# Performance work log

Hardware: AMD Instinct MI355X
Metric: run time of the kernel (lower is better)

## Reference

```python
import jax, jax.numpy as jnp
import numpy as np

EMBED_DIM = 768
NUM_HEADS = 12
SEGMENT_LENGTHS = (2048, 4096, 8192)
DILATION_RATES = (1, 2, 4)
LN_EPS = 1e-5


def setup_inputs() -> dict:
    key = jax.random.key(0)
    ks = jax.random.split(key, 12)
    B, N, E = 2, 8192, EMBED_DIM
    xavier = (2.0 / (E + E)) ** 0.5  # xavier_normal_ std for square weight
    return {
        "query": jax.random.normal(ks[0], (B, N, E), jnp.float32),
        "key_": jax.random.normal(ks[1], (B, N, E), jnp.float32),
        "value": jax.random.normal(ks[2], (B, N, E), jnp.float32),
        "Wq": jax.random.normal(ks[3], (E, E), jnp.float32) * xavier,
        "bq": jnp.zeros((E,), jnp.float32),
        "Wk": jax.random.normal(ks[4], (E, E), jnp.float32) * xavier,
        "bk": jnp.zeros((E,), jnp.float32),
        "Wv": jax.random.normal(ks[5], (E, E), jnp.float32) * xavier,
        "bv": jnp.zeros((E,), jnp.float32),
        "Wo": jax.random.normal(ks[6], (E, E), jnp.float32) * xavier,
        "bo": jnp.zeros((E,), jnp.float32),
        "ln_g": jnp.ones((E,), jnp.float32),
        "ln_b": jnp.zeros((E,), jnp.float32),
    }


def _dilated_attention(q, k, v):
    # q,k,v: [b, n, h, d]  (LongNet dilated attention, non-causal)
    b, n, h, d = q.shape
    G = len(SEGMENT_LENGTHS)
    hpg = h // G  # heads per dilation group
    scale = 1.0 / jnp.sqrt(jnp.asarray(d, q.dtype))
    out = jnp.zeros_like(q)
    for i, (g, r) in enumerate(zip(SEGMENT_LENGTHS, DILATION_RATES)):
        offset = i % r
        hmin, hmax = i * hpg, (i + 1) * hpg
        def seg(x):
            # [b, n_seg, g, h, d] -> dilate within segment, slice head group
            xs = x.reshape(b, n // g, g, h, d)
            return xs[:, :, offset::r, hmin:hmax, :]  # [b, ns, s, hg, d]
        qs, ks_, vs = seg(q), seg(k), seg(v)
        # attention within each dilated segment
        scores = jnp.einsum("bnshd,bnthd->bnhst", qs, ks_) * scale
        attn = jax.nn.softmax(scores, axis=-1)
        xo = jnp.einsum("bnhst,bnthd->bnshd", attn, vs)
        out_r = out.reshape(b, n // g, g, h, d)
        out_r = out_r.at[:, :, offset::r, hmin:hmax, :].add(xo)
        out = out_r.reshape(b, n, h, d)
    return out / G


def reference(query, key_, value, Wq, bq, Wk, bk, Wv, bv, Wo, bo, ln_g, ln_b):
    b, n, e = query.shape
    h, d = NUM_HEADS, e // NUM_HEADS
    q = (query @ Wq.T + bq).reshape(b, n, h, d)
    k = (key_ @ Wk.T + bk).reshape(b, n, h, d)
    v = (value @ Wv.T + bv).reshape(b, n, h, d)
    x = _dilated_attention(q, k, v).reshape(b, n, e)
    mu = jnp.mean(x, axis=-1, keepdims=True)
    var = jnp.mean(jnp.square(x - mu), axis=-1, keepdims=True)
    x = (x - mu) * jax.lax.rsqrt(var + LN_EPS) * ln_g + ln_b
    return x @ Wo.T + bo
```

## Files before the change

kernel.cpp:

```cpp
#include <hip/hip_runtime.h>
#include <hip/hip_bf16.h>
#include <stdint.h>

typedef unsigned int uint32;
typedef unsigned short u16;
typedef __attribute__((ext_vector_type(4))) float f32x4;
typedef __attribute__((ext_vector_type(16))) float f32x16;
typedef __attribute__((ext_vector_type(8))) __bf16 bf16x8;
typedef __attribute__((ext_vector_type(8))) short i16x8;
typedef __attribute__((ext_vector_type(4))) short i16x4;
typedef __attribute__((ext_vector_type(4))) uint32 u32x4;

#define DEVINL static __device__ __forceinline__

DEVINL u16 f2bf(float f){
  uint32 u = __builtin_bit_cast(uint32, f);
  return (u16)((u + 0x7fffu + ((u >> 16) & 1u)) >> 16);
}

DEVINL uint32 cvtpk(float lo, float hi){
  uint32 r;
  asm("v_cvt_pk_bf16_f32 %0, %1, %2" : "=v"(r) : "v"(lo), "v"(hi));
  return r;
}

DEVINL void permswap(uint32 &a, uint32 &b){
  asm volatile("s_nop 1\n\tv_permlane32_swap_b32 %0, %1" : "+v"(a), "+v"(b));
}

DEVINL f32x4 mfma16(bf16x8 a, bf16x8 b, f32x4 c){
  return __builtin_amdgcn_mfma_f32_16x16x32_bf16(a, b, c, 0, 0, 0);
}
DEVINL f32x16 mfma32(bf16x8 a, bf16x8 b, f32x16 c){
  return __builtin_amdgcn_mfma_f32_32x32x16_bf16(a, b, c, 0, 0, 0);
}
DEVINL f32x16 zero16(){
  f32x16 z;
  #pragma unroll
  for (int r = 0; r < 16; ++r) z[r] = 0.f;
  return z;
}

DEVINL void gload16(const u16* g, u16* l){
  __builtin_amdgcn_global_load_lds(
      (const __attribute__((address_space(1))) uint32*)g,
      (__attribute__((address_space(3))) uint32*)l, 16, 0, 0);
}

static constexpr int LDK = 40;
static constexpr size_t ISTR = 2048 * 64;
static constexpr float QSCALE = 0.18033688011112042f;

__global__ void cvt_w(const float* __restrict__ src, u16* __restrict__ dst, int n4){
  int i = blockIdx.x * 256 + threadIdx.x;
  if (i < n4){
    f32x4 v = *(const f32x4*)(src + (size_t)i * 4);
    u16 o[4];
    #pragma unroll
    for (int j = 0; j < 4; ++j) o[j] = f2bf(v[j]);
    *(i16x4*)(dst + (size_t)i * 4) = *(const i16x4*)o;
  }
}

__global__ __launch_bounds__(256) void qkv_gemm(
    const float* __restrict__ X, const u16* __restrict__ W,
    const float* __restrict__ bias, u16* __restrict__ Yg,
    float scale, int tmode)
{
  __shared__ u16 As[128 * LDK];
  __shared__ u16 Bs[128 * LDK];
  const int tid = threadIdx.x;
  const int l = tid & 63, w = tid >> 6;
  const int l15 = l & 15, lh = l >> 4;
  const int wr = w >> 1, wc = w & 1;
  const int row0 = blockIdx.x * 128, col0 = blockIdx.y * 128;
  const int sr = tid >> 1, skc = (tid & 1) * 16;

  const float* ap = X + (size_t)(row0 + sr) * 768 + skc;
  const u16*   bp = W + (size_t)(col0 + sr) * 768 + skc;

  f32x4 acc[4][4];
  #pragma unroll
  for (int i = 0; i < 4; ++i)
    #pragma unroll
    for (int j = 0; j < 4; ++j) acc[i][j] = f32x4{0.f, 0.f, 0.f, 0.f};

  f32x4 ra0, ra1, ra2, ra3; i16x8 rb0, rb1;
  ra0 = *(const f32x4*)(ap);      ra1 = *(const f32x4*)(ap + 4);
  ra2 = *(const f32x4*)(ap + 8);  ra3 = *(const f32x4*)(ap + 12);
  rb0 = *(const i16x8*)(bp);      rb1 = *(const i16x8*)(bp + 8);

  for (int ks = 0; ks < 24; ++ks) {
    __syncthreads();
    u32x4 w0 = { cvtpk(ra0[0], ra0[1]), cvtpk(ra0[2], ra0[3]),
                 cvtpk(ra1[0], ra1[1]), cvtpk(ra1[2], ra1[3]) };
    u32x4 w1 = { cvtpk(ra2[0], ra2[1]), cvtpk(ra2[2], ra2[3]),
                 cvtpk(ra3[0], ra3[1]), cvtpk(ra3[2], ra3[3]) };
    *(i16x8*)&As[sr * LDK + skc]     = __builtin_bit_cast(i16x8, w0);
    *(i16x8*)&As[sr * LDK + skc + 8] = __builtin_bit_cast(i16x8, w1);
    *(i16x8*)&Bs[sr * LDK + skc]     = rb0;
    *(i16x8*)&Bs[sr * LDK + skc + 8] = rb1;
    __syncthreads();
    if (ks < 23) {
      const float* ap2 = ap + (ks + 1) * 32;
      const u16*   bp2 = bp + (ks + 1) * 32;
      ra0 = *(const f32x4*)(ap2);      ra1 = *(const f32x4*)(ap2 + 4);
      ra2 = *(const f32x4*)(ap2 + 8);  ra3 = *(const f32x4*)(ap2 + 12);
      rb0 = *(const i16x8*)(bp2);      rb1 = *(const i16x8*)(bp2 + 8);
    }
    bf16x8 af[4], bfr[4];
    #pragma unroll
    for (int mi = 0; mi < 4; ++mi)
      af[mi] = *(const bf16x8*)&As[(wr * 64 + mi * 16 + l15) * LDK + lh * 8];
    #pragma unroll
    for (int ni = 0; ni < 4; ++ni)
      bfr[ni] = *(const bf16x8*)&Bs[(wc * 64 + ni * 16 + l15) * LDK + lh * 8];
    #pragma unroll
    for (int mi = 0; mi < 4; ++mi)
      #pragma unroll
      for (int ni = 0; ni < 4; ++ni)
        acc[mi][ni] = mfma16(af[mi], bfr[ni], acc[mi][ni]);
  }

  #pragma unroll
  for (int ni = 0; ni < 4; ++ni) {
    const int e = col0 + wc * 64 + ni * 16 + l15;
    const int h = e >> 6, d = e & 63;
    const int grp = h >> 2, hg = h & 3;
    const int instB = (grp == 0) ? 0 : (grp == 1) ? 32 : 48;
    const float bia = bias[e];
    #pragma unroll
    for (int mi = 0; mi < 4; ++mi) {
      #pragma unroll
      for (int r = 0; r < 4; ++r) {
        const int row = row0 + wr * 64 + mi * 16 + lh * 4 + r;
        const int b = row >> 13, nn = row & 8191;
        const int p = nn & ((2048 << grp) - 1);
        if ((p & ((1 << grp) - 1)) != grp) continue;
        const int seg = nn >> (11 + grp);
        const int t = (p - grp) >> grp;
        const int inst = instB + ((b * (4 >> grp) + seg) << 2) + hg;
        const u16 val = f2bf((acc[mi][ni][r] + bia) * scale);
        if (tmode == 0) Yg[(size_t)inst * ISTR + (size_t)t * 64 + d] = val;
        else            Yg[(size_t)inst * ISTR + (size_t)d * 2048 + t] = val;
      }
    }
  }
}

__global__ __launch_bounds__(256) void dil_attn(
    const u16* __restrict__ Qg, const u16* __restrict__ Kg,
    const u16* __restrict__ VgT, uint32* __restrict__ Op32, float* __restrict__ Ls)
{
  __shared__ u16 Kb[2][64 * 64];
  __shared__ u16 Vb[2][64 * 64];
  const int tid = threadIdx.x;
  const int w = tid >> 6, l = tid & 63;
  const int l31 = l & 31, hi = l >> 5;
  const int id = blockIdx.x;
  const int nid = (id & 7) * 224 + (id >> 3);
  const int inst = nid >> 5, rem = nid & 31;
  const int qb = rem >> 1, kh = rem & 1;
  const size_t ibase = (size_t)inst * ISTR;
  const int qbase = qb * 128 + w * 32;
  const int k0base = kh * 1024;

  const u16* qlane = Qg + ibase + (size_t)(qbase + l31) * 64 + hi * 8;
  const bf16x8 qf0 = *(const bf16x8*)(qlane);
  const bf16x8 qf1 = *(const bf16x8*)(qlane + 16);
  const bf16x8 qf2 = *(const bf16x8*)(qlane + 32);
  const bf16x8 qf3 = *(const bf16x8*)(qlane + 48);

  const int srow = l >> 3;
  const int scol = ((l & 7) ^ (srow & 7)) << 3;
  const u16* kgs = Kg  + ibase + (size_t)srow * 64 + scol;
  const u16* vgs = VgT + ibase + (size_t)srow * 2048 + scol;

  f32x16 acc0 = zero16(), acc1 = zero16(), rs = zero16();
  const int sxor = (l31 & 7) << 3;
  const bf16x8 ones = __builtin_bit_cast(bf16x8,
      u32x4{0x3F803F80u, 0x3F803F80u, 0x3F803F80u, 0x3F803F80u});

  auto STAGE = [&](int buf, int k0){
    #pragma unroll
    for (int q = 0; q < 2; ++q){
      const int rb = w * 16 + q * 8;
      gload16(kgs + (size_t)(k0 + rb) * 64, &Kb[buf][rb * 64]);
      gload16(vgs + (size_t)rb * 2048 + k0, &Vb[buf][rb * 64]);
    }
  };

  STAGE(0, k0base);
  asm volatile("s_waitcnt vmcnt(0)");
  __syncthreads();

  int cur = 0;
  for (int step = 0; step < 16; ++step) {
    if (step < 15) STAGE(cur ^ 1, k0base + ((step + 1) << 6));
    const u16* kt = &Kb[cur][0];
    const u16* vt = &Vb[cur][0];
    #pragma unroll
    for (int s = 0; s < 2; ++s) {
      const int ksub = s * 32;
      const int krow = (ksub + l31) * 64;
      bf16x8 kc0 = *(const bf16x8*)&kt[krow + ((hi * 8)      ^ sxor)];
      bf16x8 kc1 = *(const bf16x8*)&kt[krow + ((16 + hi * 8) ^ sxor)];
      bf16x8 kc2 = *(const bf16x8*)&kt[krow + ((32 + hi * 8) ^ sxor)];
      bf16x8 kc3 = *(const bf16x8*)&kt[krow + ((48 + hi * 8) ^ sxor)];

      f32x16 sT = zero16();
      sT = mfma32(kc0, qf0, sT);
      sT = mfma32(kc1, qf1, sT);
      sT = mfma32(kc2, qf2, sT);
      sT = mfma32(kc3, qf3, sT);

      #pragma unroll
      for (int r = 0; r < 16; ++r) sT[r] = __builtin_amdgcn_exp2f(sT[r]);

      uint32 cw0 = cvtpk(sT[0],  sT[1]),  cw1 = cvtpk(sT[2],  sT[3]);
      uint32 cw2 = cvtpk(sT[4],  sT[5]),  cw3 = cvtpk(sT[6],  sT[7]);
      uint32 cw4 = cvtpk(sT[8],  sT[9]),  cw5 = cvtpk(sT[10], sT[11]);
      uint32 cw6 = cvtpk(sT[12], sT[13]), cw7 = cvtpk(sT[14], sT[15]);
      permswap(cw0, cw2); permswap(cw1, cw3);
      permswap(cw4, cw6); permswap(cw5, cw7);
      bf16x8 pa0 = __builtin_bit_cast(bf16x8, u32x4{cw0, cw1, cw2, cw3});
      bf16x8 pa1 = __builtin_bit_cast(bf16x8, u32x4{cw4, cw5, cw6, cw7});

      const int vr0 = l31 * 64, vr1 = (l31 + 32) * 64;
      bf16x8 v00 = *(const bf16x8*)&vt[vr0 + ((ksub + hi * 8)      ^ sxor)];
      bf16x8 v01 = *(const bf16x8*)&vt[vr0 + ((ksub + 16 + hi * 8) ^ sxor)];
      bf16x8 v10 = *(const bf16x8*)&vt[vr1 + ((ksub + hi * 8)      ^ sxor)];
      bf16x8 v11 = *(const bf16x8*)&vt[vr1 + ((ksub + 16 + hi * 8) ^ sxor)];

      rs   = mfma32(pa0, ones, rs);
      rs   = mfma32(pa1, ones, rs);
      acc0 = mfma32(pa0, v00, acc0);
      acc0 = mfma32(pa1, v01, acc0);
      acc1 = mfma32(pa0, v10, acc1);
      acc1 = mfma32(pa1, v11, acc1);
    }
    asm volatile("s_waitcnt vmcnt(0)");
    __syncthreads();
    cur ^= 1;
  }

  if (l31 == 0) {
    float* lsp = Ls + ((size_t)kh * 56 + inst) * 2048 + qbase;
    #pragma unroll
    for (int r = 0; r < 16; ++r) {
      const int qrow = (r & 3) + 8 * (r >> 2) + 4 * hi;
      lsp[qrow] = rs[r];
    }
  }
  uint32* op = Op32 + (size_t)kh * (56u * 2048u * 32u)
                    + ((size_t)inst * 2048 + qbase) * 32 + l31;
  #pragma unroll
  for (int r = 0; r < 16; ++r) {
    const int qrow = (r & 3) + 8 * (r >> 2) + 4 * hi;
    op[(size_t)qrow * 32] = cvtpk(acc0[r], acc1[r]);
  }
}

__global__ __launch_bounds__(256) void ln_gather(
    const uint32* __restrict__ Op32, const float* __restrict__ Ls,
    const float* __restrict__ gamma, const float* __restrict__ beta,
    u16* __restrict__ xln)
{
  const int row = blockIdx.x;
  const int b = row >> 13, nn = row & 8191;
  const int tid = threadIdx.x;
  const size_t KHOFF = 56u * 2048u * 32u;
  float v[3];
  #pragma unroll
  for (int j = 0; j < 3; ++j) {
    const int e = tid + j * 256;
    const int h = e >> 6, d = e & 63;
    const int grp = h >> 2, hg = h & 3;
    const int p = nn & ((2048 << grp) - 1);
    float val = 0.f;
    if ((p & ((1 << grp) - 1)) == grp) {
      const int seg = nn >> (11 + grp);
      const int instB = (grp == 0) ? 0 : (grp == 1) ? 32 : 48;
      const int inst = instB + ((b * (4 >> grp) + seg) << 2) + hg;
      const int t = (p - grp) >> grp;
      const size_t wbase = ((size_t)inst * 2048 + t) * 32 + (d & 31);
      const uint32 w0 = Op32[wbase];
      const uint32 w1 = Op32[wbase + KHOFF];
      const float o0 = __builtin_bit_cast(float, d < 32 ? (w0 << 16) : (w0 & 0xFFFF0000u));
      const float o1 = __builtin_bit_cast(float, d < 32 ? (w1 << 16) : (w1 & 0xFFFF0000u));
      const float s = Ls[(size_t)inst * 2048 + t] + Ls[(size_t)(56 * 2048) + inst * 2048 + t];
      val = (o0 + o1) * (1.0f / (3.0f * s));
    }
    v[j] = val;
  }
  float s = v[0] + v[1] + v[2];
  float q = v[0]*v[0] + v[1]*v[1] + v[2]*v[2];
  #pragma unroll
  for (int off = 1; off < 64; off <<= 1) { s += __shfl_xor(s, off); q += __shfl_xor(q, off); }
  __shared__ float red[8];
  const int w = tid >> 6, l = tid & 63;
  if (l == 0) { red[w] = s; red[4 + w] = q; }
  __syncthreads();
  s = red[0] + red[1] + red[2] + red[3];
  q = red[4] + red[5] + red[6] + red[7];
  const float mu = s * (1.f / 768.f);
  const float var = q * (1.f / 768.f) - mu * mu;
  const float rs = rsqrtf(var + 1e-5f);
  #pragma unroll
  for (int j = 0; j < 3; ++j) {
    const int e = tid + j * 256;
    xln[(size_t)row * 768 + e] = f2bf((v[j] - mu) * rs * gamma[e] + beta[e]);
  }
}

__global__ __launch_bounds__(256) void out_gemm(
    const u16* __restrict__ Xb, const u16* __restrict__ W,
    const float* __restrict__ bias, float* __restrict__ out)
{
  __shared__ u16 As[128 * LDK];
  __shared__ u16 Bs[128 * LDK];
  const int tid = threadIdx.x;
  const int l = tid & 63, w = tid >> 6;
  const int l15 = l & 15, lh = l >> 4;
  const int wr = w >> 1, wc = w & 1;
  const int row0 = blockIdx.x * 128, col0 = blockIdx.y * 128;
  const int sr = tid >> 1, skc = (tid & 1) * 16;

  const u16* ap = Xb + (size_t)(row0 + sr) * 768 + skc;
  const u16* bp = W + (size_t)(col0 + sr) * 768 + skc;

  f32x4 acc[4][4];
  #pragma unroll
  for (int i = 0; i < 4; ++i)
    #pragma unroll
    for (int j = 0; j < 4; ++j) acc[i][j] = f32x4{0.f, 0.f, 0.f, 0.f};

  i16x8 ra0, ra1, rb0, rb1;
  ra0 = *(const i16x8*)(ap); ra1 = *(const i16x8*)(ap + 8);
  rb0 = *(const i16x8*)(bp); rb1 = *(const i16x8*)(bp + 8);

  for (int ks = 0; ks < 24; ++ks) {
    __syncthreads();
    *(i16x8*)&As[sr * LDK + skc]     = ra0;
    *(i16x8*)&As[sr * LDK + skc + 8] = ra1;
    *(i16x8*)&Bs[sr * LDK + skc]     = rb0;
    *(i16x8*)&Bs[sr * LDK + skc + 8] = rb1;
    __syncthreads();
    if (ks < 23) {
      const u16* ap2 = ap + (ks + 1) * 32;
      const u16* bp2 = bp + (ks + 1) * 32;
      ra0 = *(const i16x8*)(ap2); ra1 = *(const i16x8*)(ap2 + 8);
      rb0 = *(const i16x8*)(bp2); rb1 = *(const i16x8*)(bp2 + 8);
    }
    bf16x8 af[4], bfr[4];
    #pragma unroll
    for (int mi = 0; mi < 4; ++mi)
      af[mi] = *(const bf16x8*)&As[(wr * 64 + mi * 16 + l15) * LDK + lh * 8];
    #pragma unroll
    for (int ni = 0; ni < 4; ++ni)
      bfr[ni] = *(const bf16x8*)&Bs[(wc * 64 + ni * 16 + l15) * LDK + lh * 8];
    #pragma unroll
    for (int mi = 0; mi < 4; ++mi)
      #pragma unroll
      for (int ni = 0; ni < 4; ++ni)
        acc[mi][ni] = mfma16(af[mi], bfr[ni], acc[mi][ni]);
  }

  #pragma unroll
  for (int ni = 0; ni < 4; ++ni) {
    const int e = col0 + wc * 64 + ni * 16 + l15;
    const float bia = bias[e];
    #pragma unroll
    for (int mi = 0; mi < 4; ++mi) {
      #pragma unroll
      for (int r = 0; r < 4; ++r) {
        const int row = row0 + wr * 64 + mi * 16 + lh * 4 + r;
        out[(size_t)row * 768 + e] = acc[mi][ni][r] + bia;
      }
    }
  }
}

extern "C" void kernel_launch(void* const* d_in, const int* in_sizes, int n_in,
                              void* d_out, int out_size, void* d_ws, size_t ws_size,
                              hipStream_t stream) {
  const float* query = (const float*)d_in[0];
  const float* key_  = (const float*)d_in[1];
  const float* value = (const float*)d_in[2];
  const float* Wq = (const float*)d_in[3];
  const float* bq = (const float*)d_in[4];
  const float* Wk = (const float*)d_in[5];
  const float* bk = (const float*)d_in[6];
  const float* Wv = (const float*)d_in[7];
  const float* bv = (const float*)d_in[8];
  const float* Wo = (const float*)d_in[9];
  const float* bo = (const float*)d_in[10];
  const float* lng = (const float*)d_in[11];
  const float* lnb = (const float*)d_in[12];

  char* ws = (char*)d_ws;
  size_t off = 0;
  auto alloc = [&](size_t bytes) { size_t o = off; off += (bytes + 255) & ~(size_t)255; return o; };
  const size_t WB = 768 * 768 * 2;
  const size_t GB = (size_t)56 * ISTR * 2;
  u16* wqb = (u16*)(ws + alloc(WB));
  u16* wkb = (u16*)(ws + alloc(WB));
  u16* wvb = (u16*)(ws + alloc(WB));
  u16* wob = (u16*)(ws + alloc(WB));
  u16* Qg  = (u16*)(ws + alloc(GB));
  u16* Kg  = (u16*)(ws + alloc(GB));
  u16* VgT = (u16*)(ws + alloc(GB));
  uint32* Op32 = (uint32*)(ws + alloc((size_t)2 * 56 * 2048 * 32 * 4));
  float* Lsb  = (float*)(ws + alloc((size_t)2 * 56 * 2048 * 4));
  u16* xln = (u16*)(ws + alloc((size_t)16384 * 768 * 2));

  const int n4 = 768 * 768 / 4;
  cvt_w<<<dim3(576), 256, 0, stream>>>(Wq, wqb, n4);
  cvt_w<<<dim3(576), 256, 0, stream>>>(Wk, wkb, n4);
  cvt_w<<<dim3(576), 256, 0, stream>>>(Wv, wvb, n4);
  cvt_w<<<dim3(576), 256, 0, stream>>>(Wo, wob, n4);

  qkv_gemm<<<dim3(128, 6), 256, 0, stream>>>(query, wqb, bq, Qg, QSCALE, 0);
  qkv_gemm<<<dim3(128, 6), 256, 0, stream>>>(key_,  wkb, bk, Kg, 1.0f, 0);
  qkv_gemm<<<dim3(128, 6), 256, 0, stream>>>(value, wvb, bv, VgT, 1.0f, 1);

  dil_attn<<<dim3(1792), 256, 0, stream>>>(Qg, Kg, VgT, Op32, Lsb);
  ln_gather<<<dim3(16384), 256, 0, stream>>>(Op32, Lsb, lng, lnb, xln);
  out_gemm<<<dim3(128, 6), 256, 0, stream>>>(xln, wob, bo, (float*)d_out);
}
```

Baseline: 298.4 us.

## Double-buffer GEMM LDS with async global_load_lds and batch QKV/weight-convert launches

The QKV and output GEMMs now use double-buffered LDS tiles. Bf16 operands are staged directly into LDS with global_load_lds while the current tile is computed, and each K step needs one barrier instead of two. The three QKV projections are merged into one launch with an 18-wide grid, and the four weight conversions into one launch, to cut launch overhead and fill the GPU better. The LDS row stride drops from 40 to 32 elements with no padding, which may add bank conflicts on the fragment reads.

```diff
diff --git a/kernel.cpp b/kernel.cpp
--- a/kernel.cpp
+++ b/kernel.cpp
@@ -47,11 +47,16 @@
       (__attribute__((address_space(3))) uint32*)l, 16, 0, 0);
 }
 
-static constexpr int LDK = 40;
 static constexpr size_t ISTR = 2048 * 64;
 static constexpr float QSCALE = 0.18033688011112042f;
 
-__global__ void cvt_w(const float* __restrict__ src, u16* __restrict__ dst, int n4){
+__global__ void cvt_w4(const float* __restrict__ s0, const float* __restrict__ s1,
+                       const float* __restrict__ s2, const float* __restrict__ s3,
+                       u16* __restrict__ d0, u16* __restrict__ d1,
+                       u16* __restrict__ d2, u16* __restrict__ d3, int n4){
+  const int wsel = blockIdx.y;
+  const float* src = wsel == 0 ? s0 : wsel == 1 ? s1 : wsel == 2 ? s2 : s3;
+  u16* dst = wsel == 0 ? d0 : wsel == 1 ? d1 : wsel == 2 ? d2 : d3;
   int i = blockIdx.x * 256 + threadIdx.x;
   if (i < n4){
     f32x4 v = *(const f32x4*)(src + (size_t)i * 4);
@@ -62,22 +67,34 @@
   }
 }
 
-__global__ __launch_bounds__(256) void qkv_gemm(
-    const float* __restrict__ X, const u16* __restrict__ W,
-    const float* __restrict__ bias, u16* __restrict__ Yg,
-    float scale, int tmode)
+__global__ __launch_bounds__(256) void qkv_fused(
+    const float* __restrict__ X0, const float* __restrict__ X1, const float* __restrict__ X2,
+    const u16* __restrict__ W0, const u16* __restrict__ W1, const u16* __restrict__ W2,
+    const float* __restrict__ b0, const float* __restrict__ b1, const float* __restrict__ b2,
+    u16* __restrict__ Y0, u16* __restrict__ Y1, u16* __restrict__ Y2)
 {
-  __shared__ u16 As[128 * LDK];
-  __shared__ u16 Bs[128 * LDK];
+  __shared__ u16 As[2][128 * 32];
+  __shared__ u16 Bs[2][128 * 32];
   const int tid = threadIdx.x;
   const int l = tid & 63, w = tid >> 6;
   const int l15 = l & 15, lh = l >> 4;
   const int wr = w >> 1, wc = w & 1;
-  const int row0 = blockIdx.x * 128, col0 = blockIdx.y * 128;
-  const int sr = tid >> 1, skc = (tid & 1) * 16;
-
-  const float* ap = X + (size_t)(row0 + sr) * 768 + skc;
-  const u16*   bp = W + (size_t)(col0 + sr) * 768 + skc;
+  const int yb = blockIdx.y;
+  const int sect = yb / 6;
+  const int row0 = blockIdx.x * 128, col0 = (yb % 6) * 128;
+
+  const float* X   = sect == 0 ? X0 : sect == 1 ? X1 : X2;
+  const u16*   W   = sect == 0 ? W0 : sect == 1 ? W1 : W2;
+  const float* bia_p = sect == 0 ? b0 : sect == 1 ? b1 : b2;
+  u16*         Yg  = sect == 0 ? Y0 : sect == 1 ? Y1 : Y2;
+  const float scale = sect == 0 ? QSCALE : 1.0f;
+  const int tmode = (sect == 2) ? 1 : 0;
+
+  const int gr = l >> 2, gc = (l & 3) * 8;
+  const u16* wsrc0 = W + (size_t)(col0 + w * 32 + gr) * 768 + gc;
+
+  const int sr = tid >> 1, sc = (tid & 1) * 16;
+  const float* asrc = X + (size_t)(row0 + sr) * 768 + sc;
 
   f32x4 acc[4][4];
   #pragma unroll
@@ -85,41 +102,58 @@
     #pragma unroll
     for (int j = 0; j < 4; ++j) acc[i][j] = f32x4{0.f, 0.f, 0.f, 0.f};
 
-  f32x4 ra0, ra1, ra2, ra3; i16x8 rb0, rb1;
-  ra0 = *(const f32x4*)(ap);      ra1 = *(const f32x4*)(ap + 4);
-  ra2 = *(const f32x4*)(ap + 8);  ra3 = *(const f32x4*)(ap + 12);
-  rb0 = *(const i16x8*)(bp);      rb1 = *(const i16x8*)(bp + 8);
-
-  for (int ks = 0; ks < 24; ++ks) {
-    __syncthreads();
+  auto STAGE_B = [&](int buf, int ks){
+    const u16* ws = wsrc0 + ks * 32;
+    gload16(ws,            &Bs[buf][(w * 32) * 32]);
+    gload16(ws + 16 * 768, &Bs[buf][(w * 32 + 16) * 32]);
+  };
+  auto WRITE_A = [&](int buf, f32x4 ra0, f32x4 ra1, f32x4 ra2, f32x4 ra3){
     u32x4 w0 = { cvtpk(ra0[0], ra0[1]), cvtpk(ra0[2], ra0[3]),
                  cvtpk(ra1[0], ra1[1]), cvtpk(ra1[2], ra1[3]) };
     u32x4 w1 = { cvtpk(ra2[0], ra2[1]), cvtpk(ra2[2], ra2[3]),
                  cvtpk(ra3[0], ra3[1]), cvtpk(ra3[2], ra3[3]) };
-    *(i16x8*)&As[sr * LDK + skc]     = __builtin_bit_cast(i16x8, w0);
-    *(i16x8*)&As[sr * LDK + skc + 8] = __builtin_bit_cast(i16x8, w1);
-    *(i16x8*)&Bs[sr * LDK + skc]     = rb0;
-    *(i16x8*)&Bs[sr * LDK + skc + 8] = rb1;
-    __syncthreads();
-    if (ks < 23) {
-      const float* ap2 = ap + (ks + 1) * 32;
-      const u16*   bp2 = bp + (ks + 1) * 32;
-      ra0 = *(const f32x4*)(ap2);      ra1 = *(const f32x4*)(ap2 + 4);
-      ra2 = *(const f32x4*)(ap2 + 8);  ra3 = *(const f32x4*)(ap2 + 12);
-      rb0 = *(const i16x8*)(bp2);      rb1 = *(const i16x8*)(bp2 + 8);
+    *(i16x8*)&As[buf][sr * 32 + sc]     = __builtin_bit_cast(i16x8, w0);
+    *(i16x8*)&As[buf][sr * 32 + sc + 8] = __builtin_bit_cast(i16x8, w1);
+  };
+
+  {
+    STAGE_B(0, 0);
+    f32x4 ra0 = *(const f32x4*)(asrc);
+    f32x4 ra1 = *(const f32x4*)(asrc + 4);
+    f32x4 ra2 = *(const f32x4*)(asrc + 8);
+    f32x4 ra3 = *(const f32x4*)(asrc + 12);
+    WRITE_A(0, ra0, ra1, ra2, ra3);
+  }
+  asm volatile("s_waitcnt vmcnt(0)");
+  __syncthreads();
+
+  int cur = 0;
+  for (int ks = 0; ks < 24; ++ks) {
+    const int nxt = cur ^ 1;
+    f32x4 ra0, ra1, ra2, ra3;
+    const bool has = ks < 23;
+    if (has) {
+      STAGE_B(nxt, ks + 1);
+      const float* ap = asrc + (ks + 1) * 32;
+      ra0 = *(const f32x4*)(ap);      ra1 = *(const f32x4*)(ap + 4);
+      ra2 = *(const f32x4*)(ap + 8);  ra3 = *(const f32x4*)(ap + 12);
     }
     bf16x8 af[4], bfr[4];
     #pragma unroll
     for (int mi = 0; mi < 4; ++mi)
-      af[mi] = *(const bf16x8*)&As[(wr * 64 + mi * 16 + l15) * LDK + lh * 8];
+      af[mi] = *(const bf16x8*)&As[cur][(wr * 64 + mi * 16 + l15) * 32 + lh * 8];
     #pragma unroll
     for (int ni = 0; ni < 4; ++ni)
-      bfr[ni] = *(const bf16x8*)&Bs[(wc * 64 + ni * 16 + l15) * LDK + lh * 8];
+      bfr[ni] = *(const bf16x8*)&Bs[cur][(wc * 64 + ni * 16 + l15) * 32 + lh * 8];
     #pragma unroll
     for (int mi = 0; mi < 4; ++mi)
       #pragma unroll
       for (int ni = 0; ni < 4; ++ni)
         acc[mi][ni] = mfma16(af[mi], bfr[ni], acc[mi][ni]);
+    if (has) WRITE_A(nxt, ra0, ra1, ra2, ra3);
+    asm volatile("s_waitcnt vmcnt(0)");
+    __syncthreads();
+    cur = nxt;
   }
 
   #pragma unroll
@@ -128,7 +162,7 @@
     const int h = e >> 6, d = e & 63;
     const int grp = h >> 2, hg = h & 3;
     const int instB = (grp == 0) ? 0 : (grp == 1) ? 32 : 48;
-    const float bia = bias[e];
+    const float bia = bia_p[e];
     #pragma unroll
     for (int mi = 0; mi < 4; ++mi) {
       #pragma unroll
@@ -317,17 +351,17 @@
     const u16* __restrict__ Xb, const u16* __restrict__ W,
     const float* __restrict__ bias, float* __restrict__ out)
 {
-  __shared__ u16 As[128 * LDK];
-  __shared__ u16 Bs[128 * LDK];
+  __shared__ u16 As[2][128 * 32];
+  __shared__ u16 Bs[2][128 * 32];
   const int tid = threadIdx.x;
   const int l = tid & 63, w = tid >> 6;
   const int l15 = l & 15, lh = l >> 4;
   const int wr = w >> 1, wc = w & 1;
   const int row0 = blockIdx.x * 128, col0 = blockIdx.y * 128;
-  const int sr = tid >> 1, skc = (tid & 1) * 16;
-
-  const u16* ap = Xb + (size_t)(row0 + sr) * 768 + skc;
-  const u16* bp = W + (size_t)(col0 + sr) * 768 + skc;
+
+  const int gr = l >> 2, gc = (l & 3) * 8;
+  const u16* asrc0 = Xb + (size_t)(row0 + w * 32 + gr) * 768 + gc;
+  const u16* wsrc0 = W  + (size_t)(col0 + w * 32 + gr) * 768 + gc;
 
   f32x4 acc[4][4];
   #pragma unroll
@@ -335,35 +369,38 @@
     #pragma unroll
     for (int j = 0; j < 4; ++j) acc[i][j] = f32x4{0.f, 0.f, 0.f, 0.f};
 
-  i16x8 ra0, ra1, rb0, rb1;
-  ra0 = *(const i16x8*)(ap); ra1 = *(const i16x8*)(ap + 8);
-  rb0 = *(const i16x8*)(bp); rb1 = *(const i16x8*)(bp + 8);
-
+  auto STAGE = [&](int buf, int ks){
+    const u16* as = asrc0 + ks * 32;
+    const u16* ws = wsrc0 + ks * 32;
+    gload16(as,            &As[buf][(w * 32) * 32]);
+    gload16(as + 16 * 768, &As[buf][(w * 32 + 16) * 32]);
+    gload16(ws,            &Bs[buf][(w * 32) * 32]);
+    gload16(ws + 16 * 768, &Bs[buf][(w * 32 + 16) * 32]);
+  };
+
+  STAGE(0, 0);
+  asm volatile("s_waitcnt vmcnt(0)");
+  __syncthreads();
+
+  int cur = 0;
   for (int ks = 0; ks < 24; ++ks) {
-    __syncthreads();
-    *(i16x8*)&As[sr * LDK + skc]     = ra0;
-    *(i16x8*)&As[sr * LDK + skc + 8] = ra1;
-    *(i16x8*)&Bs[sr * LDK + skc]     = rb0;
-    *(i16x8*)&Bs[sr * LDK + skc + 8] = rb1;
-    __syncthreads();
-    if (ks < 23) {
-      const u16* ap2 = ap + (ks + 1) * 32;
-      const u16* bp2 = bp + (ks + 1) * 32;
-      ra0 = *(const i16x8*)(ap2); ra1 = *(const i16x8*)(ap2 + 8);
-      rb0 = *(const i16x8*)(bp2); rb1 = *(const i16x8*)(bp2 + 8);
-    }
+    const int nxt = cur ^ 1;
+    if (ks < 23) STAGE(nxt, ks + 1);
     bf16x8 af[4], bfr[4];
     #pragma unroll
     for (int mi = 0; mi < 4; ++mi)
-      af[mi] = *(const bf16x8*)&As[(wr * 64 + mi * 16 + l15) * LDK + lh * 8];
+      af[mi] = *(const bf16x8*)&As[cur][(wr * 64 + mi * 16 + l15) * 32 + lh * 8];
     #pragma unroll
     for (int ni = 0; ni < 4; ++ni)
-      bfr[ni] = *(const bf16x8*)&Bs[(wc * 64 + ni * 16 + l15) * LDK + lh * 8];
+      bfr[ni] = *(const bf16x8*)&Bs[cur][(wc * 64 + ni * 16 + l15) * 32 + lh * 8];
     #pragma unroll
     for (int mi = 0; mi < 4; ++mi)
       #pragma unroll
       for (int ni = 0; ni < 4; ++ni)
         acc[mi][ni] = mfma16(af[mi], bfr[ni], acc[mi][ni]);
+    asm volatile("s_waitcnt vmcnt(0)");
+    __syncthreads();
+    cur = nxt;
   }
 
   #pragma unroll
@@ -415,14 +452,10 @@
   u16* xln = (u16*)(ws + alloc((size_t)16384 * 768 * 2));
 
   const int n4 = 768 * 768 / 4;
-  cvt_w<<<dim3(576), 256, 0, stream>>>(Wq, wqb, n4);
-  cvt_w<<<dim3(576), 256, 0, stream>>>(Wk, wkb, n4);
-  cvt_w<<<dim3(576), 256, 0, stream>>>(Wv, wvb, n4);
-  cvt_w<<<dim3(576), 256, 0, stream>>>(Wo, wob, n4);
-
-  qkv_gemm<<<dim3(128, 6), 256, 0, stream>>>(query, wqb, bq, Qg, QSCALE, 0);
-  qkv_gemm<<<dim3(128, 6), 256, 0, stream>>>(key_,  wkb, bk, Kg, 1.0f, 0);
-  qkv_gemm<<<dim3(128, 6), 256, 0, stream>>>(value, wvb, bv, VgT, 1.0f, 1);
+  cvt_w4<<<dim3(576, 4), 256, 0, stream>>>(Wq, Wk, Wv, Wo, wqb, wkb, wvb, wob, n4);
+
+  qkv_fused<<<dim3(128, 18), 256, 0, stream>>>(
+      query, key_, value, wqb, wkb, wvb, bq, bk, bv, Qg, Kg, VgT);
 
   dil_attn<<<dim3(1792), 256, 0, stream>>>(Qg, Kg, VgT, Op32, Lsb);
   ln_gather<<<dim3(16384), 256, 0, stream>>>(Op32, Lsb, lng, lnb, xln);
```

After: 287.6 us. 1.04x faster.
